# Kernel optimization log

Measured on AMD Instinct MI355X. Metric: run time of the kernel, lower is better.

Reference implementation:

```python
import jax, jax.numpy as jnp
import numpy as np

N_NODES = 1_000_000
N_GRAPHS = 8192
DIM = 64
FEAT = 64


def setup_inputs() -> dict:
    key = jax.random.key(0)
    ks = jax.random.split(key, 12)
    s = 0.05
    inp = {}
    inp["x"] = jax.random.normal(ks[0], (N_NODES, FEAT), jnp.float32)
    inp["batch"] = jnp.sort(jax.random.randint(ks[1], (N_NODES,), 0, N_GRAPHS, dtype=jnp.int32))
    inp["lin0_w"] = jax.random.normal(ks[2], (DIM, FEAT), jnp.float32) * s
    inp["lin0_b"] = jnp.zeros((DIM,), jnp.float32)
    inp["lin1_w"] = jax.random.normal(ks[3], (DIM, DIM), jnp.float32) * s
    inp["lin1_b"] = jnp.zeros((DIM,), jnp.float32)
    inp["gru_wih"] = jax.random.normal(ks[4], (3 * DIM, DIM), jnp.float32) * s
    inp["gru_whh"] = jax.random.normal(ks[5], (3 * DIM, DIM), jnp.float32) * s
    inp["gru_bih"] = jnp.zeros((3 * DIM,), jnp.float32)
    inp["gru_bhh"] = jnp.zeros((3 * DIM,), jnp.float32)
    inp["lstm_wih"] = jax.random.normal(ks[6], (4 * DIM, 2 * DIM), jnp.float32) * s
    inp["lstm_whh"] = jax.random.normal(ks[7], (4 * DIM, DIM), jnp.float32) * s
    inp["lstm_bih"] = jnp.zeros((4 * DIM,), jnp.float32)
    inp["lstm_bhh"] = jnp.zeros((4 * DIM,), jnp.float32)
    inp["lin2_w"] = jax.random.normal(ks[8], (DIM, 2 * DIM), jnp.float32) * s
    inp["lin2_b"] = jnp.zeros((DIM,), jnp.float32)
    inp["lin3_w"] = jax.random.normal(ks[9], (1, DIM), jnp.float32) * s
    inp["lin3_b"] = jnp.zeros((1,), jnp.float32)
    inp["n_graphs"] = N_GRAPHS
    return inp


def _gru_step(m, h, wih, whh, bih, bhh):
    # single-step PyTorch GRU semantics
    gi = m @ wih.T + bih          # [N, 3D]
    gh = h @ whh.T + bhh          # [N, 3D]
    ir, iz, in_ = jnp.split(gi, 3, axis=-1)
    hr, hz, hn = jnp.split(gh, 3, axis=-1)
    r = jax.nn.sigmoid(ir + hr)
    z = jax.nn.sigmoid(iz + hz)
    n = jnp.tanh(in_ + r * hn)
    return (1.0 - z) * n + z * h


def _segment_softmax(e, batch, n_graphs):
    m = jax.ops.segment_max(e, batch, num_segments=n_graphs)
    ex = jnp.exp(e - m[batch])
    s = jax.ops.segment_sum(ex, batch, num_segments=n_graphs)
    return ex / (s[batch] + 1e-16)


def reference(x, batch, lin0_w, lin0_b, lin1_w, lin1_b,
              gru_wih, gru_whh, gru_bih, gru_bhh,
              lstm_wih, lstm_whh, lstm_bih, lstm_bhh,
              lin2_w, lin2_b, lin3_w, lin3_b, n_graphs):
    dim = lin0_w.shape[0]
    out = jax.nn.relu(x @ lin0_w.T + lin0_b)   # [N, D]
    h = out
    for _ in range(3):
        m = jax.nn.relu(out @ lin1_w.T + lin1_b)
        h = _gru_step(m, h, gru_wih, gru_whh, gru_bih, gru_bhh)
        out = h

    # Set2Set, processing_steps = 3
    q_star = jnp.zeros((n_graphs, 2 * dim), out.dtype)
    hl = jnp.zeros((n_graphs, dim), out.dtype)
    cl = jnp.zeros((n_graphs, dim), out.dtype)
    for _ in range(3):
        gates = q_star @ lstm_wih.T + lstm_bih + hl @ lstm_whh.T + lstm_bhh  # [B, 4D]
        gi, gf, gg, go = jnp.split(gates, 4, axis=-1)
        cl = jax.nn.sigmoid(gf) * cl + jax.nn.sigmoid(gi) * jnp.tanh(gg)
        hl = jax.nn.sigmoid(go) * jnp.tanh(cl)
        q = hl                                   # [B, D]
        e = jnp.sum(out * q[batch], axis=-1)     # [N]
        a = _segment_softmax(e, batch, n_graphs) # [N]
        r = jax.ops.segment_sum(a[:, None] * out, batch, num_segments=n_graphs)  # [B, D]
        q_star = jnp.concatenate([q, r], axis=-1)

    y = jax.nn.relu(q_star @ lin2_w.T + lin2_b)
    y = y @ lin3_w.T + lin3_b
    return y.reshape(-1)
```

## Files before the change

kernel.cpp:

```cpp
#include <hip/hip_runtime.h>
#include <hip/hip_bf16.h>
#include <math.h>

#define TILES 8
#define MBLK 128

typedef __attribute__((ext_vector_type(8))) short bf8;
typedef __attribute__((ext_vector_type(4))) float f32x4;

#define MFMA(a, b, c) __builtin_amdgcn_mfma_f32_16x16x32_bf16(a, b, c, 0, 0, 0)

__device__ __forceinline__ float fast_rcp(float x) { return __builtin_amdgcn_rcpf(x); }
__device__ __forceinline__ float sigm(float x) { return fast_rcp(1.0f + __expf(-x)); }
__device__ __forceinline__ float tanh2(float x) { return fmaf(2.0f, fast_rcp(1.0f + __expf(-2.0f * x)), -1.0f); }

__device__ __forceinline__ unsigned short f2bf(float v) {
    union { __hip_bfloat16 b; unsigned short u; } cv;
    cv.b = __float2bfloat16(v);
    return cv.u;
}
__device__ __forceinline__ float bf2f(unsigned short u) {
    union { unsigned short u; __hip_bfloat16 b; } cv;
    cv.u = u;
    return __bfloat162float(cv.b);
}
__device__ __forceinline__ f32x4 ntload4(const float* p) {
    return __builtin_nontemporal_load((const f32x4*)p);
}

__global__ void prep_kernel(const float* __restrict__ l0w, const float* __restrict__ l1w,
                            const float* __restrict__ gwih, const float* __restrict__ gwhh,
                            const float* __restrict__ lwih, const float* __restrict__ lwhh,
                            const float* __restrict__ l2w,
                            const int* __restrict__ batch,
                            unsigned short* __restrict__ whi, unsigned short* __restrict__ wlo,
                            float* __restrict__ liT, float* __restrict__ lhT,
                            float* __restrict__ l2T,
                            float* __restrict__ u, float* __restrict__ cl,
                            int* __restrict__ startp,
                            int n_nodes, int n_graphs)
{
    int tid = blockIdx.x * 256 + threadIdx.x;
    int nthreads = gridDim.x * 256;
    if (tid < 32768) {
        int e = tid & 7, lane = (tid >> 3) & 63, ks = (tid >> 9) & 1, jt = tid >> 10;
        const float* W; int jl;
        if (jt < 4)       { W = l0w;  jl = jt; }
        else if (jt < 8)  { W = l1w;  jl = jt - 4; }
        else if (jt < 20) { W = gwih; jl = jt - 8; }
        else              { W = gwhh; jl = jt - 20; }
        int j = jl * 16 + (lane & 15);
        int k = ks * 32 + (lane >> 4) * 8 + e;
        float v = W[j * 64 + k];
        unsigned short hi = f2bf(v);
        whi[tid] = hi;
        wlo[tid] = f2bf(v - bf2f(hi));
    }
    if (tid < 32768) liT[tid] = lwih[(tid & 255) * 128 + (tid >> 8)];
    if (tid < 16384) lhT[tid] = lwhh[(tid & 255) * 64 + (tid >> 8)];
    if (tid < 8192)  l2T[tid] = l2w[(tid & 63) * 128 + (tid >> 6)];
    if (tid <= n_graphs) {
        int lo = 0, hi = n_nodes;
        while (lo < hi) {
            int mid = (lo + hi) >> 1;
            if (batch[mid] < tid) lo = mid + 1; else hi = mid;
        }
        startp[tid] = lo;
    }
    for (int i = tid; i < n_graphs * 192; i += nthreads) u[i] = 0.0f;
    for (int i = tid; i < n_graphs * 64;  i += nthreads) cl[i] = 0.0f;
}

__launch_bounds__(256, 2)
__global__ void node_kernel(const float* __restrict__ x,
                            const unsigned short* __restrict__ whi,
                            const unsigned short* __restrict__ wlo,
                            const float* __restrict__ l0b, const float* __restrict__ l1b,
                            const float* __restrict__ gbih, const float* __restrict__ gbhh,
                            float* __restrict__ outv, int n_nodes)
{
    __shared__ unsigned short MHI[8192], MLO[8192], HHI[8192], HLO[8192];
    const int tid = threadIdx.x;
    const int w = tid >> 6, lane = tid & 63, c = lane & 15, g = lane >> 4;
    const long node0 = (long)blockIdx.x * MBLK;
    const int j = w * 16 + c;

    const float bR  = gbih[j] + gbhh[j];
    const float bZ  = gbih[64 + j] + gbhh[64 + j];
    const float bNI = gbih[128 + j];
    const float bNH = gbhh[128 + j];
    const float bL1 = l1b[j];
    const float bL0 = l0b[j];

    const int koff = ((j >> 5) * 512) + (((j >> 3) & 3) * 128) + (j & 7);

    const bf8* WH = (const bf8*)whi;
    const bf8* WL = (const bf8*)wlo;
#define LF(name, jt) \
    bf8 name##h0 = WH[((jt) * 2 + 0) * 64 + lane], name##h1 = WH[((jt) * 2 + 1) * 64 + lane], \
        name##l0 = WL[((jt) * 2 + 0) * 64 + lane], name##l1 = WL[((jt) * 2 + 1) * 64 + lane];
    LF(w0, w)
    LF(w1, 4 + w)
    LF(gir, 8 + w)  LF(giz, 12 + w)  LF(gin, 16 + w)
    LF(ghr, 20 + w) LF(ghz, 24 + w) LF(ghn, 28 + w)
#undef LF

    float hc[TILES][4];

#pragma unroll
    for (int t = 0; t < TILES; ++t) {
        long nd = node0 + t * 16 + c;
        if (nd >= n_nodes) nd = n_nodes - 1;
        const float* xp = x + nd * 64 + g * 8;
        float va[8], vb[8];
        {
            float4 u0 = *(const float4*)xp;
            float4 u1 = *(const float4*)(xp + 4);
            float4 u2 = *(const float4*)(xp + 32);
            float4 u3 = *(const float4*)(xp + 36);
            va[0] = u0.x; va[1] = u0.y; va[2] = u0.z; va[3] = u0.w;
            va[4] = u1.x; va[5] = u1.y; va[6] = u1.z; va[7] = u1.w;
            vb[0] = u2.x; vb[1] = u2.y; vb[2] = u2.z; vb[3] = u2.w;
            vb[4] = u3.x; vb[5] = u3.y; vb[6] = u3.z; vb[7] = u3.w;
        }
        bf8 xh0, xl0, xh1, xl1;
#pragma unroll
        for (int e = 0; e < 8; ++e) {
            unsigned short h0 = f2bf(va[e]);
            xh0[e] = (short)h0; xl0[e] = (short)f2bf(va[e] - bf2f(h0));
            unsigned short h1 = f2bf(vb[e]);
            xh1[e] = (short)h1; xl1[e] = (short)f2bf(vb[e] - bf2f(h1));
        }
        f32x4 acc = {bL0, bL0, bL0, bL0};
        acc = MFMA(xh0, w0h0, acc); acc = MFMA(xl0, w0h0, acc); acc = MFMA(xh0, w0l0, acc);
        acc = MFMA(xh1, w0h1, acc); acc = MFMA(xl1, w0h1, acc); acc = MFMA(xh1, w0l1, acc);
#pragma unroll
        for (int p = 0; p < 4; ++p) {
            float hv = fmaxf(acc[p], 0.0f);
            hc[t][p] = hv;
            int r = g * 4 + p;
            unsigned short hi = f2bf(hv);
            HHI[t * 1024 + koff + r * 8] = hi;
            HLO[t * 1024 + koff + r * 8] = f2bf(hv - bf2f(hi));
        }
    }
    __syncthreads();

    for (int iter = 0; iter < 3; ++iter) {
#pragma unroll
        for (int t = 0; t < TILES; ++t) {
            const bf8* hh = (const bf8*)&HHI[t * 1024];
            const bf8* hl = (const bf8*)&HLO[t * 1024];
            bf8 ah0 = hh[lane], ah1 = hh[64 + lane];
            bf8 al0 = hl[lane], al1 = hl[64 + lane];
            f32x4 acc = {bL1, bL1, bL1, bL1};
            acc = MFMA(ah0, w1h0, acc); acc = MFMA(al0, w1h0, acc); acc = MFMA(ah0, w1l0, acc);
            acc = MFMA(ah1, w1h1, acc); acc = MFMA(al1, w1h1, acc); acc = MFMA(ah1, w1l1, acc);
#pragma unroll
            for (int p = 0; p < 4; ++p) {
                float mv = fmaxf(acc[p], 0.0f);
                int r = g * 4 + p;
                unsigned short hi = f2bf(mv);
                MHI[t * 1024 + koff + r * 8] = hi;
                MLO[t * 1024 + koff + r * 8] = f2bf(mv - bf2f(hi));
            }
        }
        __syncthreads();

#pragma unroll
        for (int t = 0; t < TILES; ++t) {
            const bf8* mh = (const bf8*)&MHI[t * 1024];
            const bf8* ml = (const bf8*)&MLO[t * 1024];
            const bf8* hh = (const bf8*)&HHI[t * 1024];
            const bf8* hl = (const bf8*)&HLO[t * 1024];
            bf8 amh0 = mh[lane], amh1 = mh[64 + lane];
            bf8 aml0 = ml[lane], aml1 = ml[64 + lane];
            bf8 ahh0 = hh[lane], ahh1 = hh[64 + lane];
            bf8 ahl0 = hl[lane], ahl1 = hl[64 + lane];

            f32x4 aR  = {bR, bR, bR, bR};
            f32x4 aZ  = {bZ, bZ, bZ, bZ};
            f32x4 aNI = {bNI, bNI, bNI, bNI};
            f32x4 aNH = {bNH, bNH, bNH, bNH};

            aR = MFMA(amh0, girh0, aR); aR = MFMA(aml0, girh0, aR); aR = MFMA(amh0, girl0, aR);
            aR = MFMA(amh1, girh1, aR); aR = MFMA(aml1, girh1, aR); aR = MFMA(amh1, girl1, aR);
            aR = MFMA(ahh0, ghrh0, aR); aR = MFMA(ahl0, ghrh0, aR); aR = MFMA(ahh0, ghrl0, aR);
            aR = MFMA(ahh1, ghrh1, aR); aR = MFMA(ahl1, ghrh1, aR); aR = MFMA(ahh1, ghrl1, aR);

            aZ = MFMA(amh0, gizh0, aZ); aZ = MFMA(aml0, gizh0, aZ); aZ = MFMA(amh0, gizl0, aZ);
            aZ = MFMA(amh1, gizh1, aZ); aZ = MFMA(aml1, gizh1, aZ); aZ = MFMA(amh1, gizl1, aZ);
            aZ = MFMA(ahh0, ghzh0, aZ); aZ = MFMA(ahl0, ghzh0, aZ); aZ = MFMA(ahh0, ghzl0, aZ);
            aZ = MFMA(ahh1, ghzh1, aZ); aZ = MFMA(ahl1, ghzh1, aZ); aZ = MFMA(ahh1, ghzl1, aZ);

            aNI = MFMA(amh0, ginh0, aNI); aNI = MFMA(aml0, ginh0, aNI); aNI = MFMA(amh0, ginl0, aNI);
            aNI = MFMA(amh1, ginh1, aNI); aNI = MFMA(aml1, ginh1, aNI); aNI = MFMA(amh1, ginl1, aNI);

            aNH = MFMA(ahh0, ghnh0, aNH); aNH = MFMA(ahl0, ghnh0, aNH); aNH = MFMA(ahh0, ghnl0, aNH);
            aNH = MFMA(ahh1, ghnh1, aNH); aNH = MFMA(ahl1, ghnh1, aNH); aNH = MFMA(ahh1, ghnl1, aNH);

#pragma unroll
            for (int p = 0; p < 4; ++p) {
                float rg = sigm(aR[p]);
                float zg = sigm(aZ[p]);
                float ng = tanh2(aNI[p] + rg * aNH[p]);
                hc[t][p] = (1.0f - zg) * ng + zg * hc[t][p];
            }
        }

        if (iter < 2) {
            __syncthreads();
#pragma unroll
            for (int t = 0; t < TILES; ++t)
#pragma unroll
                for (int p = 0; p < 4; ++p) {
                    int r = g * 4 + p;
                    unsigned short hi = f2bf(hc[t][p]);
                    HHI[t * 1024 + koff + r * 8] = hi;
                    HLO[t * 1024 + koff + r * 8] = f2bf(hc[t][p] - bf2f(hi));
                }
            __syncthreads();
        }
    }

#pragma unroll
    for (int t = 0; t < TILES; ++t)
#pragma unroll
        for (int p = 0; p < 4; ++p) {
            long nd = node0 + t * 16 + g * 4 + p;
            if (nd < n_nodes) outv[nd * 64 + j] = hc[t][p];
        }
}

__global__ void lstm_kernel(const float* __restrict__ liT, const float* __restrict__ lhT,
                            const float* __restrict__ lbih, const float* __restrict__ lbhh,
                            float* __restrict__ u, float* __restrict__ cl, int n_graphs)
{
    const int t = threadIdx.x;
    const int g = blockIdx.x * 4 + (t >> 6);
    const int d = t & 63;
    if (g >= n_graphs) return;
    float* ug = u + (size_t)g * 192;

    float aI = lbih[d]       + lbhh[d];
    float aF = lbih[64 + d]  + lbhh[64 + d];
    float aG = lbih[128 + d] + lbhh[128 + d];
    float aO = lbih[192 + d] + lbhh[192 + d];
    for (int k = 0; k < 128; ++k) {
        float uv = ug[k];
        const float* wr = liT + k * 256;
        aI = fmaf(wr[d], uv, aI);
        aF = fmaf(wr[64 + d], uv, aF);
        aG = fmaf(wr[128 + d], uv, aG);
        aO = fmaf(wr[192 + d], uv, aO);
    }
    for (int k = 0; k < 64; ++k) {
        float hv = ug[128 + k];
        const float* wr = lhT + k * 256;
        aI = fmaf(wr[d], hv, aI);
        aF = fmaf(wr[64 + d], hv, aF);
        aG = fmaf(wr[128 + d], hv, aG);
        aO = fmaf(wr[192 + d], hv, aO);
    }
    float c = sigm(aF) * cl[(size_t)g * 64 + d] + sigm(aI) * tanh2(aG);
    cl[(size_t)g * 64 + d] = c;
    float h = sigm(aO) * tanh2(c);
    ug[d] = h;
    ug[128 + d] = h;
}

__global__ void attn_kernel(const float* __restrict__ outv,
                            const int* __restrict__ startp,
                            float* __restrict__ u, int n_graphs)
{
    __shared__ float qS[64];
    __shared__ float mG[16], sG[16];
    __shared__ float rG[16][64];

    const int g = blockIdx.x;
    const int t = threadIdx.x;
    const int s0 = startp[g];
    const int cnt = startp[g + 1] - s0;
    if (t < 64) qS[t] = u[(size_t)g * 192 + t];
    __syncthreads();

    const int grp = t >> 4, l = t & 15;
    const float q0 = qS[l * 4], q1 = qS[l * 4 + 1], q2 = qS[l * 4 + 2], q3 = qS[l * 4 + 3];

    float m = -INFINITY, s = 0.0f;
    float r0 = 0.0f, r1 = 0.0f, r2 = 0.0f, r3 = 0.0f;

    int n = grp;
    for (; n + 16 < cnt; n += 32) {
        f32x4 va = ntload4(outv + (size_t)(s0 + n) * 64 + l * 4);
        f32x4 vb = ntload4(outv + (size_t)(s0 + n + 16) * 64 + l * 4);
        float ea = fmaf(va.x, q0, fmaf(va.y, q1, fmaf(va.z, q2, va.w * q3)));
        float eb = fmaf(vb.x, q0, fmaf(vb.y, q1, fmaf(vb.z, q2, vb.w * q3)));
#pragma unroll
        for (int o = 1; o < 16; o <<= 1) {
            ea += __shfl_xor(ea, o);
            eb += __shfl_xor(eb, o);
        }
        float mn = fmaxf(m, fmaxf(ea, eb));
        float sc = __expf(m - mn);
        float wa = __expf(ea - mn);
        float wb = __expf(eb - mn);
        s = s * sc + wa + wb;
        r0 = fmaf(r0, sc, fmaf(wa, va.x, wb * vb.x));
        r1 = fmaf(r1, sc, fmaf(wa, va.y, wb * vb.y));
        r2 = fmaf(r2, sc, fmaf(wa, va.z, wb * vb.z));
        r3 = fmaf(r3, sc, fmaf(wa, va.w, wb * vb.w));
        m = mn;
    }
    if (n < cnt) {
        f32x4 va = ntload4(outv + (size_t)(s0 + n) * 64 + l * 4);
        float ea = fmaf(va.x, q0, fmaf(va.y, q1, fmaf(va.z, q2, va.w * q3)));
#pragma unroll
        for (int o = 1; o < 16; o <<= 1) ea += __shfl_xor(ea, o);
        float mn = fmaxf(m, ea);
        float sc = __expf(m - mn);
        float wa = __expf(ea - mn);
        s = s * sc + wa;
        r0 = fmaf(r0, sc, wa * va.x);
        r1 = fmaf(r1, sc, wa * va.y);
        r2 = fmaf(r2, sc, wa * va.z);
        r3 = fmaf(r3, sc, wa * va.w);
        m = mn;
    }

    if (l == 0) { mG[grp] = m; sG[grp] = s; }
    rG[grp][l * 4 + 0] = r0;
    rG[grp][l * 4 + 1] = r1;
    rG[grp][l * 4 + 2] = r2;
    rG[grp][l * 4 + 3] = r3;
    __syncthreads();

    if (t < 64) {
        float M = -INFINITY;
#pragma unroll
        for (int j2 = 0; j2 < 16; ++j2) M = fmaxf(M, mG[j2]);
        float out;
        if (M == -INFINITY) {
            out = 0.0f;
        } else {
            float ssum = 0.0f, racc = 0.0f;
#pragma unroll
            for (int j2 = 0; j2 < 16; ++j2) {
                float sc = __expf(mG[j2] - M);
                ssum = fmaf(sG[j2], sc, ssum);
                racc = fmaf(rG[j2][t], sc, racc);
            }
            out = racc / (ssum + 1e-16f);
        }
        u[(size_t)g * 192 + 64 + t] = out;
    }
}

__global__ void head_kernel(const float* __restrict__ u,
                            const float* __restrict__ l2T, const float* __restrict__ l2b,
                            const float* __restrict__ l3w, const float* __restrict__ l3b,
                            float* __restrict__ yout, int n_graphs)
{
    const int t = threadIdx.x;
    const int g = blockIdx.x * 4 + (t >> 6);
    const int d = t & 63;
    if (g >= n_graphs) return;
    const float* ug = u + (size_t)g * 192;
    float a0 = l2b[d], a1 = 0.0f, a2 = 0.0f, a3 = 0.0f;
    for (int k = 0; k < 128; k += 4) {
        a0 = fmaf(l2T[(k + 0) * 64 + d], ug[k + 0], a0);
        a1 = fmaf(l2T[(k + 1) * 64 + d], ug[k + 1], a1);
        a2 = fmaf(l2T[(k + 2) * 64 + d], ug[k + 2], a2);
        a3 = fmaf(l2T[(k + 3) * 64 + d], ug[k + 3], a3);
    }
    float y = fmaxf((a0 + a1) + (a2 + a3), 0.0f);
    float p = l3w[d] * y;
#pragma unroll
    for (int o = 32; o > 0; o >>= 1) p += __shfl_xor(p, o);
    if (d == 0) yout[g] = p + l3b[0];
}

extern "C" void kernel_launch(void* const* d_in, const int* in_sizes, int n_in,
                              void* d_out, int out_size, void* d_ws, size_t ws_size,
                              hipStream_t stream)
{
    const float* x     = (const float*)d_in[0];
    const int*   batch = (const int*)d_in[1];
    const float* l0w   = (const float*)d_in[2];
    const float* l0b   = (const float*)d_in[3];
    const float* l1w   = (const float*)d_in[4];
    const float* l1b   = (const float*)d_in[5];
    const float* gwih  = (const float*)d_in[6];
    const float* gwhh  = (const float*)d_in[7];
    const float* gbih  = (const float*)d_in[8];
    const float* gbhh  = (const float*)d_in[9];
    const float* lwih  = (const float*)d_in[10];
    const float* lwhh  = (const float*)d_in[11];
    const float* lbih  = (const float*)d_in[12];
    const float* lbhh  = (const float*)d_in[13];
    const float* l2w   = (const float*)d_in[14];
    const float* l2b   = (const float*)d_in[15];
    const float* l3w   = (const float*)d_in[16];
    const float* l3b   = (const float*)d_in[17];

    const int n_nodes  = in_sizes[1];
    const int n_graphs = out_size;

    float* wsf = (float*)d_ws;
    float* outv = wsf;
    float* liT  = wsf + (size_t)n_nodes * 64;
    float* lhT  = liT + 32768;
    float* l2T  = lhT + 16384;
    unsigned short* whi = (unsigned short*)(l2T + 8192);
    unsigned short* wlo = whi + 32768;
    float* u    = (float*)(wlo + 32768);
    float* cl   = u + (size_t)n_graphs * 192;
    int* startp = (int*)(cl + (size_t)n_graphs * 64);

    prep_kernel<<<768, 256, 0, stream>>>(l0w, l1w, gwih, gwhh, lwih, lwhh, l2w, batch,
                                         whi, wlo, liT, lhT, l2T, u, cl, startp,
                                         n_nodes, n_graphs);
    node_kernel<<<(n_nodes + MBLK - 1) / MBLK, 256, 0, stream>>>(
        x, whi, wlo, l0b, l1b, gbih, gbhh, outv, n_nodes);
    for (int step = 0; step < 3; ++step) {
        lstm_kernel<<<(n_graphs + 3) / 4, 256, 0, stream>>>(liT, lhT, lbih, lbhh,
                                                            u, cl, n_graphs);
        attn_kernel<<<n_graphs, 256, 0, stream>>>(outv, startp, u, n_graphs);
    }
    head_kernel<<<(n_graphs + 3) / 4, 256, 0, stream>>>(u, l2T, l2b, l3w, l3b,
                                                        (float*)d_out, n_graphs);
}
```

Before: 853.9 us.

## Halve node tile, XOR-swizzle LDS layout, and truncate for bf16 hi split

Halves the nodes per block from 128 to 64 and the per-block LDS use, and raises launch bounds to 4 blocks per CU to get more occupancy. Adds an XOR swizzle on the LDS row index to cut bank conflicts on the scattered bf16 stores and on the fragment reads. Replaces round-to-nearest for the high bf16 half with bit truncation, which makes the hi/lo split cheaper. The risks are register spills under the tighter launch bound, more blocks each reloading the weight fragments, and a small change in rounding of the split.

New measurement: 2.580 ms. 3.02x slower.

```diff
diff --git a/kernel.cpp b/kernel.cpp
--- a/kernel.cpp
+++ b/kernel.cpp
@@ -2,8 +2,8 @@
 #include <hip/hip_bf16.h>
 #include <math.h>
 
-#define TILES 8
-#define MBLK 128
+#define TILES 4
+#define MBLK 64
 
 typedef __attribute__((ext_vector_type(8))) short bf8;
 typedef __attribute__((ext_vector_type(4))) float f32x4;
@@ -23,6 +23,12 @@
     union { unsigned short u; __hip_bfloat16 b; } cv;
     cv.u = u;
     return __bfloat162float(cv.b);
+}
+__device__ __forceinline__ void split_tr(float v, unsigned short& hi, unsigned short& lo) {
+    unsigned int uv = __builtin_bit_cast(unsigned int, v);
+    hi = (unsigned short)(uv >> 16);
+    float rem = v - __builtin_bit_cast(float, uv & 0xffff0000u);
+    lo = f2bf(rem);
 }
 __device__ __forceinline__ f32x4 ntload4(const float* p) {
     return __builtin_nontemporal_load((const f32x4*)p);
@@ -71,7 +77,7 @@
     for (int i = tid; i < n_graphs * 64;  i += nthreads) cl[i] = 0.0f;
 }
 
-__launch_bounds__(256, 2)
+__launch_bounds__(256, 4)
 __global__ void node_kernel(const float* __restrict__ x,
                             const unsigned short* __restrict__ whi,
                             const unsigned short* __restrict__ wlo,
@@ -79,7 +85,7 @@
                             const float* __restrict__ gbih, const float* __restrict__ gbhh,
                             float* __restrict__ outv, int n_nodes)
 {
-    __shared__ unsigned short MHI[8192], MLO[8192], HHI[8192], HLO[8192];
+    __shared__ unsigned short MHI[4096], MLO[4096], HHI[4096], HLO[4096];
     const int tid = threadIdx.x;
     const int w = tid >> 6, lane = tid & 63, c = lane & 15, g = lane >> 4;
     const long node0 = (long)blockIdx.x * MBLK;
@@ -92,7 +98,9 @@
     const float bL1 = l1b[j];
     const float bL0 = l0b[j];
 
-    const int koff = ((j >> 5) * 512) + (((j >> 3) & 3) * 128) + (j & 7);
+    const int kgj = (j >> 3) & 3;
+    const int koff2 = ((j >> 5) * 512) + (kgj * 128) + (j & 7);
+    const int lane_swz = (lane & 48) | (c ^ g);
 
     const bf8* WH = (const bf8*)whi;
     const bf8* WL = (const bf8*)wlo;
@@ -126,10 +134,11 @@
         bf8 xh0, xl0, xh1, xl1;
 #pragma unroll
         for (int e = 0; e < 8; ++e) {
-            unsigned short h0 = f2bf(va[e]);
-            xh0[e] = (short)h0; xl0[e] = (short)f2bf(va[e] - bf2f(h0));
-            unsigned short h1 = f2bf(vb[e]);
-            xh1[e] = (short)h1; xl1[e] = (short)f2bf(vb[e] - bf2f(h1));
+            unsigned short h0, l0, h1, l1;
+            split_tr(va[e], h0, l0);
+            split_tr(vb[e], h1, l1);
+            xh0[e] = (short)h0; xl0[e] = (short)l0;
+            xh1[e] = (short)h1; xl1[e] = (short)l1;
         }
         f32x4 acc = {bL0, bL0, bL0, bL0};
         acc = MFMA(xh0, w0h0, acc); acc = MFMA(xl0, w0h0, acc); acc = MFMA(xh0, w0l0, acc);
@@ -139,9 +148,11 @@
             float hv = fmaxf(acc[p], 0.0f);
             hc[t][p] = hv;
             int r = g * 4 + p;
-            unsigned short hi = f2bf(hv);
-            HHI[t * 1024 + koff + r * 8] = hi;
-            HLO[t * 1024 + koff + r * 8] = f2bf(hv - bf2f(hi));
+            unsigned short hi, lo;
+            split_tr(hv, hi, lo);
+            int idx = t * 1024 + koff2 + ((r ^ kgj) << 3);
+            HHI[idx] = hi;
+            HLO[idx] = lo;
         }
     }
     __syncthreads();
@@ -151,8 +162,8 @@
         for (int t = 0; t < TILES; ++t) {
             const bf8* hh = (const bf8*)&HHI[t * 1024];
             const bf8* hl = (const bf8*)&HLO[t * 1024];
-            bf8 ah0 = hh[lane], ah1 = hh[64 + lane];
-            bf8 al0 = hl[lane], al1 = hl[64 + lane];
+            bf8 ah0 = hh[lane_swz], ah1 = hh[64 + lane_swz];
+            bf8 al0 = hl[lane_swz], al1 = hl[64 + lane_swz];
             f32x4 acc = {bL1, bL1, bL1, bL1};
             acc = MFMA(ah0, w1h0, acc); acc = MFMA(al0, w1h0, acc); acc = MFMA(ah0, w1l0, acc);
             acc = MFMA(ah1, w1h1, acc); acc = MFMA(al1, w1h1, acc); acc = MFMA(ah1, w1l1, acc);
@@ -160,9 +171,11 @@
             for (int p = 0; p < 4; ++p) {
                 float mv = fmaxf(acc[p], 0.0f);
                 int r = g * 4 + p;
-                unsigned short hi = f2bf(mv);
-                MHI[t * 1024 + koff + r * 8] = hi;
-                MLO[t * 1024 + koff + r * 8] = f2bf(mv - bf2f(hi));
+                unsigned short hi, lo;
+                split_tr(mv, hi, lo);
+                int idx = t * 1024 + koff2 + ((r ^ kgj) << 3);
+                MHI[idx] = hi;
+                MLO[idx] = lo;
             }
         }
         __syncthreads();
@@ -173,10 +186,10 @@
             const bf8* ml = (const bf8*)&MLO[t * 1024];
             const bf8* hh = (const bf8*)&HHI[t * 1024];
             const bf8* hl = (const bf8*)&HLO[t * 1024];
-            bf8 amh0 = mh[lane], amh1 = mh[64 + lane];
-            bf8 aml0 = ml[lane], aml1 = ml[64 + lane];
-            bf8 ahh0 = hh[lane], ahh1 = hh[64 + lane];
-            bf8 ahl0 = hl[lane], ahl1 = hl[64 + lane];
+            bf8 amh0 = mh[lane_swz], amh1 = mh[64 + lane_swz];
+            bf8 aml0 = ml[lane_swz], aml1 = ml[64 + lane_swz];
+            bf8 ahh0 = hh[lane_swz], ahh1 = hh[64 + lane_swz];
+            bf8 ahl0 = hl[lane_swz], ahl1 = hl[64 + lane_swz];
 
             f32x4 aR  = {bR, bR, bR, bR};
             f32x4 aZ  = {bZ, bZ, bZ, bZ};
@@ -215,9 +228,11 @@
 #pragma unroll
                 for (int p = 0; p < 4; ++p) {
                     int r = g * 4 + p;
-                    unsigned short hi = f2bf(hc[t][p]);
-                    HHI[t * 1024 + koff + r * 8] = hi;
-                    HLO[t * 1024 + koff + r * 8] = f2bf(hc[t][p] - bf2f(hi));
+                    unsigned short hi, lo;
+                    split_tr(hc[t][p], hi, lo);
+                    int idx = t * 1024 + koff2 + ((r ^ kgj) << 3);
+                    HHI[idx] = hi;
+                    HLO[idx] = lo;
                 }
             __syncthreads();
         }
```
